# Kernel optimization log

Hardware: AMD Instinct MI355X
Metric: run time of the kernel (lower is better)

## Reference

```python
import jax, jax.numpy as jnp
import numpy as np

RES = 32


def _normalize_coords(coords, R):
    # coords: [B, 3, N] -> norm_coords in [0, R-1] (PVCNN Voxelization, normalize=True, eps=0)
    c = coords - coords.mean(axis=2, keepdims=True)
    scale = jnp.linalg.norm(c, axis=1, keepdims=True).max(axis=2, keepdims=True) * 2.0  # [B,1,1]
    c = c / scale + 0.5
    return jnp.clip(c * R, 0.0, R - 1.0)


def avg_voxelize(features, coords, R):
    # features: [B, C, N], coords: [B, 3, N] -> vox [B, C, R^3], norm_coords [B, 3, N]
    norm_coords = _normalize_coords(coords, R)
    vc = jnp.round(norm_coords).astype(jnp.int32)  # [B, 3, N]
    flat = (vc[:, 0] * R + vc[:, 1]) * R + vc[:, 2]  # [B, N]

    def per_batch(f, idx):
        sums = jax.ops.segment_sum(f.T, idx, num_segments=R ** 3)  # [R^3, C]
        cnt = jax.ops.segment_sum(jnp.ones(idx.shape, f.dtype), idx, num_segments=R ** 3)  # [R^3]
        return (sums / jnp.maximum(cnt, 1.0)[:, None]).T  # [C, R^3]

    vox = jax.vmap(per_batch)(features, flat)
    return vox, norm_coords


def trilinear_devoxelize(vox, coords, R):
    # vox: [B, C, R^3], coords: [B, 3, N] floats in [0, R-1]
    B, C, _ = vox.shape
    N = coords.shape[2]
    lo_f = jnp.floor(coords)
    d = coords - lo_f  # fractional part [B, 3, N]
    lo = lo_f.astype(jnp.int32)
    hi = jnp.minimum(lo + 1, R - 1)
    out = jnp.zeros((B, C, N), vox.dtype)
    for dx in (0, 1):
        for dy in (0, 1):
            for dz in (0, 1):
                ix = hi[:, 0] if dx else lo[:, 0]
                iy = hi[:, 1] if dy else lo[:, 1]
                iz = hi[:, 2] if dz else lo[:, 2]
                wx = d[:, 0] if dx else 1.0 - d[:, 0]
                wy = d[:, 1] if dy else 1.0 - d[:, 1]
                wz = d[:, 2] if dz else 1.0 - d[:, 2]
                w = wx * wy * wz  # [B, N]
                idx = (ix * R + iy) * R + iz  # [B, N]
                g = jnp.take_along_axis(vox, jnp.broadcast_to(idx[:, None, :], (B, C, N)), axis=2)
                out = out + w[:, None, :] * g
    return out


def setup_inputs() -> dict:
    key = jax.random.key(0)
    k1, k2, k3, k4 = jax.random.split(key, 4)
    B, C, N = 8, 64, 65536
    return {
        'x1_features': jax.random.normal(k1, (B, C, N), jnp.float32),
        'x2_features': jax.random.normal(k2, (B, C, N), jnp.float32),
        'x1_coords': jax.random.uniform(k3, (B, 3, N), jnp.float32),
        'x2_coords': jax.random.uniform(k4, (B, 3, N), jnp.float32),
    }


def reference(x1_features, x2_features, x1_coords, x2_coords):
    R = RES
    _vox_x1, nc_x1 = avg_voxelize(x1_features, x1_coords, R)
    vox_x2, _nc_x2 = avg_voxelize(x2_features, x2_coords, R)
    devox_mixed = trilinear_devoxelize(vox_x2, nc_x1, R)
    return jnp.concatenate([x1_features, devox_mixed], axis=1)
```

## Files before the change

kernel.cpp:

```cpp
#include <hip/hip_runtime.h>

namespace {
constexpr int R   = 32;
constexpr int R3  = R * R * R;
constexpr int NB  = 8;
constexpr int NC  = 64;
constexpr int NP  = 65536;

constexpr size_t OFF_SUM = 0;
constexpr size_t OFF_MAX = 512;
constexpr size_t OFF_CNT = 1024;
constexpr size_t OFF_VOX = OFF_CNT + sizeof(float) * (size_t)NB * R3;
constexpr size_t WS_BYTES = OFF_VOX + sizeof(float) * (size_t)NB * R3 * NC;

typedef float vfloat4 __attribute__((ext_vector_type(4)));
}

__device__ inline double wave_sum(double v) {
#pragma unroll
  for (int o = 32; o > 0; o >>= 1) v += __shfl_down(v, o, 64);
  return v;
}
__device__ inline double wave_max(double v) {
#pragma unroll
  for (int o = 32; o > 0; o >>= 1) v = fmax(v, __shfl_down(v, o, 64));
  return v;
}

__global__ __launch_bounds__(256) void k_sum(const float* __restrict__ c1,
                                             const float* __restrict__ c2,
                                             double* __restrict__ sums) {
  constexpr int CH = 32;
  int blk = blockIdx.x;
  int chunk = blk % CH; blk /= CH;
  int axis  = blk % 3;  blk /= 3;
  int b     = blk % NB; blk /= NB;
  int set   = blk;
  const float* src = (set == 0 ? c1 : c2) + ((size_t)b * 3 + axis) * NP;
  constexpr int PER = NP / CH;
  int base = chunk * PER;
  double s = 0.0;
  for (int i = threadIdx.x; i < PER; i += 256) s += (double)src[base + i];
  s = wave_sum(s);
  __shared__ double red[4];
  if ((threadIdx.x & 63) == 0) red[threadIdx.x >> 6] = s;
  __syncthreads();
  if (threadIdx.x == 0) {
    double t = red[0] + red[1] + red[2] + red[3];
    atomicAdd(&sums[((size_t)set * NB + b) * 3 + axis], t);
  }
}

__global__ __launch_bounds__(256) void k_max(const float* __restrict__ c1,
                                             const float* __restrict__ c2,
                                             const double* __restrict__ sums,
                                             unsigned long long* __restrict__ maxs) {
  constexpr int CH = 64;
  int blk = blockIdx.x;
  int chunk = blk % CH; blk /= CH;
  int b     = blk % NB; blk /= NB;
  int set   = blk;
  const float* src = (set == 0 ? c1 : c2) + (size_t)b * 3 * NP;
  const double invN = 1.0 / (double)NP;
  double m0 = sums[((size_t)set * NB + b) * 3 + 0] * invN;
  double m1 = sums[((size_t)set * NB + b) * 3 + 1] * invN;
  double m2 = sums[((size_t)set * NB + b) * 3 + 2] * invN;
  constexpr int PER = NP / CH;
  int base = chunk * PER;
  double mx = 0.0;
  for (int i = threadIdx.x; i < PER; i += 256) {
    int p = base + i;
    double x = (double)src[p] - m0;
    double y = (double)src[NP + p] - m1;
    double z = (double)src[2 * NP + p] - m2;
    mx = fmax(mx, x * x + y * y + z * z);
  }
  mx = wave_max(mx);
  __shared__ double red[4];
  if ((threadIdx.x & 63) == 0) red[threadIdx.x >> 6] = mx;
  __syncthreads();
  if (threadIdx.x == 0) {
    double t = fmax(fmax(red[0], red[1]), fmax(red[2], red[3]));
    atomicMax(&maxs[set * NB + b], (unsigned long long)__double_as_longlong(t));
  }
}

__global__ __launch_bounds__(256) void k_vox(const float* __restrict__ f2,
                                             const float* __restrict__ c2,
                                             const float* __restrict__ f1,
                                             const double* __restrict__ sums,
                                             const unsigned long long* __restrict__ maxs,
                                             float* __restrict__ counts,
                                             float* __restrict__ vox,
                                             float* __restrict__ out) {
  int lin = blockIdx.x;
  int b = lin & 7;
  int t = lin >> 3;
  int q = t / 5, r = t - q * 5;
  int tid = threadIdx.x;

  if (r == 4) {
    int p0c = q * 256;
    int w = tid >> 6, lane = tid & 63;
    const vfloat4* s4 = (const vfloat4*)(f1 + (size_t)b * NC * NP + p0c);
    vfloat4*       d4 = (vfloat4*)(out + (size_t)b * 2 * NC * NP + p0c);
#pragma unroll
    for (int rr = 0; rr < 16; ++rr) {
      int c = w * 16 + rr;
      size_t off = (size_t)c * (NP / 4) + lane;
      __builtin_nontemporal_store(__builtin_nontemporal_load(s4 + off), d4 + off);
    }
    return;
  }

  int p0 = (q * 4 + r) * 64;
  __shared__ int   s_idx[64];
  __shared__ float s_tile[64 * 65];

  if (tid < 64) {
    int p = p0 + tid;
    const double invN = 1.0 / (double)NP;
    double scale = 2.0 * sqrt(__longlong_as_double((long long)maxs[NB + b]));
    double inv = 1.0 / scale;
    const float* cb = c2 + (size_t)b * 3 * NP;
    int vc[3];
#pragma unroll
    for (int a = 0; a < 3; a++) {
      double mean = sums[((size_t)NB + b) * 3 + a] * invN;
      double nc = (((double)cb[a * NP + p] - mean) * inv + 0.5) * (double)R;
      nc = fmin(fmax(nc, 0.0), (double)(R - 1));
      vc[a] = (int)rint(nc);
    }
    int idx = (vc[0] * R + vc[1]) * R + vc[2];
    s_idx[tid] = idx;
    atomicAdd(&counts[(size_t)b * R3 + idx], 1.0f);
  }
  __syncthreads();

  const float* fb = f2 + (size_t)b * NC * NP;
#pragma unroll
  for (int i = 0; i < 16; i++) {
    int lin2 = i * 256 + tid;
    int c = lin2 >> 6, pl = lin2 & 63;
    s_tile[pl * 65 + c] = __builtin_nontemporal_load(&fb[(size_t)c * NP + p0 + pl]);
  }
  __syncthreads();

  int w = tid >> 6, lane = tid & 63;
  float* voxb = vox + (size_t)b * R3 * NC;
  for (int j = 0; j < 16; j++) {
    int pl = w * 16 + j;
    atomicAdd(&voxb[(size_t)s_idx[pl] * NC + lane], s_tile[pl * 65 + lane]);
  }
}

__global__ __launch_bounds__(256) void k_devox(const float* __restrict__ c1,
                                               const double* __restrict__ sums,
                                               const unsigned long long* __restrict__ maxs,
                                               const float* __restrict__ counts,
                                               const float* __restrict__ vox,
                                               float* __restrict__ out) {
  int lin = blockIdx.x;
  int b = lin & 7;
  int p0 = (lin >> 3) * 64;
  __shared__ int   s_idx[64][8];
  __shared__ float s_w[64][8];
  __shared__ float s_tile[64 * 65];
  int tid = threadIdx.x;

  if (tid < 64) {
    int p = p0 + tid;
    const double invN = 1.0 / (double)NP;
    double scale = 2.0 * sqrt(__longlong_as_double((long long)maxs[b]));
    double inv = 1.0 / scale;
    const float* cb = c1 + (size_t)b * 3 * NP;
    double nc[3];
#pragma unroll
    for (int a = 0; a < 3; a++) {
      double mean = sums[(size_t)b * 3 + a] * invN;
      double v = (((double)cb[a * NP + p] - mean) * inv + 0.5) * (double)R;
      nc[a] = fmin(fmax(v, 0.0), (double)(R - 1));
    }
    int lo[3], hi[3];
    double d[3];
#pragma unroll
    for (int a = 0; a < 3; a++) {
      lo[a] = (int)floor(nc[a]);
      d[a]  = nc[a] - (double)lo[a];
      hi[a] = min(lo[a] + 1, R - 1);
    }
    const float* cntb = counts + (size_t)b * R3;
#pragma unroll
    for (int k = 0; k < 8; k++) {
      int ix = (k & 4) ? hi[0] : lo[0];
      int iy = (k & 2) ? hi[1] : lo[1];
      int iz = (k & 1) ? hi[2] : lo[2];
      double wx = (k & 4) ? d[0] : 1.0 - d[0];
      double wy = (k & 2) ? d[1] : 1.0 - d[1];
      double wz = (k & 1) ? d[2] : 1.0 - d[2];
      int idx = (ix * R + iy) * R + iz;
      float cnt = cntb[idx];
      s_idx[tid][k] = idx;
      s_w[tid][k]   = (float)(wx * wy * wz) / fmaxf(cnt, 1.0f);
    }
  }
  __syncthreads();

  const float* voxb = vox + (size_t)b * R3 * NC;
  int w = tid >> 6, lane = tid & 63;
  for (int j = 0; j < 16; j++) {
    int pl = w * 16 + j;
    float acc = 0.0f;
#pragma unroll
    for (int k = 0; k < 8; k++) {
      acc += s_w[pl][k] * voxb[(size_t)s_idx[pl][k] * NC + lane];
    }
    s_tile[pl * 65 + lane] = acc;
  }
  __syncthreads();

  float* outb = out + (size_t)b * (2 * NC) * NP;
#pragma unroll
  for (int i = 0; i < 16; i++) {
    int lin2 = i * 256 + tid;
    int c = lin2 >> 6, pl = lin2 & 63;
    size_t pcol = (size_t)p0 + pl;
    __builtin_nontemporal_store(s_tile[pl * 65 + c], &outb[(size_t)(NC + c) * NP + pcol]);
  }
}

extern "C" void kernel_launch(void* const* d_in, const int* in_sizes, int n_in,
                              void* d_out, int out_size, void* d_ws, size_t ws_size,
                              hipStream_t stream) {
  const float* x1f = (const float*)d_in[0];
  const float* x2f = (const float*)d_in[1];
  const float* x1c = (const float*)d_in[2];
  const float* x2c = (const float*)d_in[3];
  float* out = (float*)d_out;

  char* ws = (char*)d_ws;
  double* sums             = (double*)(ws + OFF_SUM);
  unsigned long long* maxs = (unsigned long long*)(ws + OFF_MAX);
  float* cnts              = (float*)(ws + OFF_CNT);
  float* vox               = (float*)(ws + OFF_VOX);

  (void)hipMemsetAsync(ws, 0, WS_BYTES, stream);
  k_sum<<<2 * NB * 3 * 32, 256, 0, stream>>>(x1c, x2c, sums);
  k_max<<<2 * NB * 64, 256, 0, stream>>>(x1c, x2c, sums, maxs);
  k_vox<<<NB * (NP / 64 + NP / 256), 256, 0, stream>>>(x2f, x2c, x1f, sums, maxs, cnts, vox, out);
  k_devox<<<NB * (NP / 64), 256, 0, stream>>>(x1c, sums, maxs, cnts, vox, out);
}
```

Before: 585.1 us.

## Replace atomic voxel accumulation with counting-sort scatter and per-voxel reduction

Voxelization no longer uses float atomicAdd into the voxel grid. The new path computes voxel indices and integer counts, prefix-scans the counts per batch, scatters point features into voxel-sorted order, and then sums each voxel's contiguous run to produce the mean. The averaging moves into the reduce step, and the x1 feature copy moves into the devox kernel. This aims to cut atomic contention on hot voxels, at the cost of an extra 128MB write plus read of the sorted feature buffer, more kernel launches, and a serial per-voxel loop that is imbalanced when voxel counts are skewed.

```diff
diff --git a/kernel.cpp b/kernel.cpp
--- a/kernel.cpp
+++ b/kernel.cpp
@@ -10,8 +10,12 @@
 constexpr size_t OFF_SUM = 0;
 constexpr size_t OFF_MAX = 512;
 constexpr size_t OFF_CNT = 1024;
-constexpr size_t OFF_VOX = OFF_CNT + sizeof(float) * (size_t)NB * R3;
-constexpr size_t WS_BYTES = OFF_VOX + sizeof(float) * (size_t)NB * R3 * NC;
+constexpr size_t OFF_OFF = OFF_CNT + sizeof(int) * (size_t)NB * R3;
+constexpr size_t OFF_CUR = OFF_OFF + sizeof(int) * (size_t)NB * R3;
+constexpr size_t OFF_IDX = OFF_CUR + sizeof(int) * (size_t)NB * R3;
+constexpr size_t OFF_VOX = OFF_IDX + sizeof(int) * (size_t)NB * NP;
+constexpr size_t OFF_FT  = OFF_VOX + sizeof(float) * (size_t)NB * R3 * NC;
+constexpr size_t WS_BYTES = OFF_FT + sizeof(float) * (size_t)NB * NP * NC;
 
 typedef float vfloat4 __attribute__((ext_vector_type(4)));
 }
@@ -85,14 +89,122 @@
   }
 }
 
-__global__ __launch_bounds__(256) void k_vox(const float* __restrict__ f2,
-                                             const float* __restrict__ c2,
-                                             const float* __restrict__ f1,
+__global__ __launch_bounds__(256) void k_idx(const float* __restrict__ c2,
                                              const double* __restrict__ sums,
                                              const unsigned long long* __restrict__ maxs,
-                                             float* __restrict__ counts,
-                                             float* __restrict__ vox,
-                                             float* __restrict__ out) {
+                                             int* __restrict__ counts,
+                                             int* __restrict__ idxArr) {
+  int lin = blockIdx.x;
+  int b = lin & 7;
+  int p0 = (lin >> 3) * 1024;
+  const double invN = 1.0 / (double)NP;
+  double scale = 2.0 * sqrt(__longlong_as_double((long long)maxs[NB + b]));
+  double inv = 1.0 / scale;
+  double m0 = sums[((size_t)NB + b) * 3 + 0] * invN;
+  double m1 = sums[((size_t)NB + b) * 3 + 1] * invN;
+  double m2 = sums[((size_t)NB + b) * 3 + 2] * invN;
+  const float* cb = c2 + (size_t)b * 3 * NP;
+#pragma unroll
+  for (int k = 0; k < 4; k++) {
+    int p = p0 + k * 256 + threadIdx.x;
+    double n0 = (((double)cb[p] - m0) * inv + 0.5) * (double)R;
+    double n1 = (((double)cb[NP + p] - m1) * inv + 0.5) * (double)R;
+    double n2 = (((double)cb[2 * NP + p] - m2) * inv + 0.5) * (double)R;
+    n0 = fmin(fmax(n0, 0.0), (double)(R - 1));
+    n1 = fmin(fmax(n1, 0.0), (double)(R - 1));
+    n2 = fmin(fmax(n2, 0.0), (double)(R - 1));
+    int id = ((int)rint(n0) * R + (int)rint(n1)) * R + (int)rint(n2);
+    idxArr[(size_t)b * NP + p] = id;
+    atomicAdd(&counts[(size_t)b * R3 + id], 1);
+  }
+}
+
+__global__ __launch_bounds__(1024) void k_prefix(const int* __restrict__ counts,
+                                                 int* __restrict__ offs,
+                                                 int* __restrict__ cur) {
+  int b = blockIdx.x;
+  int t = threadIdx.x;
+  int lane = t & 63, w = t >> 6;
+  __shared__ int wtot[16];
+  int base = b * R3 + t * 32;
+  int c[32]; int s = 0;
+#pragma unroll
+  for (int k = 0; k < 32; k++) { c[k] = counts[base + k]; s += c[k]; }
+  int v = s;
+#pragma unroll
+  for (int o = 1; o < 64; o <<= 1) { int u = __shfl_up(v, o, 64); if (lane >= o) v += u; }
+  if (lane == 63) wtot[w] = v;
+  __syncthreads();
+  if (w == 0) {
+    int x = (lane < 16) ? wtot[lane] : 0;
+#pragma unroll
+    for (int o = 1; o < 16; o <<= 1) { int u = __shfl_up(x, o, 64); if (lane >= o) x += u; }
+    if (lane < 16) wtot[lane] = x;
+  }
+  __syncthreads();
+  int run = v - s + (w > 0 ? wtot[w - 1] : 0);
+#pragma unroll
+  for (int k = 0; k < 32; k++) { offs[base + k] = run; cur[base + k] = run; run += c[k]; }
+}
+
+__global__ __launch_bounds__(256) void k_scatter(const float* __restrict__ f2,
+                                                 const int* __restrict__ idxArr,
+                                                 int* __restrict__ cur,
+                                                 float* __restrict__ fT) {
+  int lin = blockIdx.x;
+  int b = lin & 7;
+  int p0 = (lin >> 3) * 64;
+  int tid = threadIdx.x;
+  __shared__ int   s_pos[64];
+  __shared__ float s_tile[64 * 65];
+
+  if (tid < 64) {
+    int id = idxArr[(size_t)b * NP + p0 + tid];
+    s_pos[tid] = atomicAdd(&cur[(size_t)b * R3 + id], 1);
+  }
+  __syncthreads();
+
+  const float* fb = f2 + (size_t)b * NC * NP;
+#pragma unroll
+  for (int i = 0; i < 16; i++) {
+    int l2 = i * 256 + tid;
+    int c = l2 >> 6, pl = l2 & 63;
+    s_tile[pl * 65 + c] = __builtin_nontemporal_load(&fb[(size_t)c * NP + p0 + pl]);
+  }
+  __syncthreads();
+
+  int w = tid >> 6, lane = tid & 63;
+  float* ftb = fT + (size_t)b * NP * NC;
+  for (int j = 0; j < 16; j++) {
+    int pl = w * 16 + j;
+    ftb[(size_t)s_pos[pl] * NC + lane] = s_tile[pl * 65 + lane];
+  }
+}
+
+__global__ __launch_bounds__(256) void k_reduce(const int* __restrict__ counts,
+                                                const int* __restrict__ offs,
+                                                const float* __restrict__ fT,
+                                                float* __restrict__ vox) {
+  int lin = blockIdx.x;
+  int b = lin & 7;
+  int v = (lin >> 3) * 4 + (threadIdx.x >> 6);
+  int lane = threadIdx.x & 63;
+  int off = offs[(size_t)b * R3 + v];
+  int cnt = counts[(size_t)b * R3 + v];
+  const float* ftb = fT + (size_t)b * NP * NC;
+  float acc = 0.0f;
+  for (int i = 0; i < cnt; i++)
+    acc += __builtin_nontemporal_load(&ftb[(size_t)(off + i) * NC + lane]);
+  float m = (cnt > 0) ? acc / (float)cnt : 0.0f;
+  vox[((size_t)b * R3 + v) * NC + lane] = m;
+}
+
+__global__ __launch_bounds__(256) void k_devox(const float* __restrict__ c1,
+                                               const double* __restrict__ sums,
+                                               const unsigned long long* __restrict__ maxs,
+                                               const float* __restrict__ vox,
+                                               const float* __restrict__ f1,
+                                               float* __restrict__ out) {
   int lin = blockIdx.x;
   int b = lin & 7;
   int t = lin >> 3;
@@ -114,59 +226,9 @@
   }
 
   int p0 = (q * 4 + r) * 64;
-  __shared__ int   s_idx[64];
-  __shared__ float s_tile[64 * 65];
-
-  if (tid < 64) {
-    int p = p0 + tid;
-    const double invN = 1.0 / (double)NP;
-    double scale = 2.0 * sqrt(__longlong_as_double((long long)maxs[NB + b]));
-    double inv = 1.0 / scale;
-    const float* cb = c2 + (size_t)b * 3 * NP;
-    int vc[3];
-#pragma unroll
-    for (int a = 0; a < 3; a++) {
-      double mean = sums[((size_t)NB + b) * 3 + a] * invN;
-      double nc = (((double)cb[a * NP + p] - mean) * inv + 0.5) * (double)R;
-      nc = fmin(fmax(nc, 0.0), (double)(R - 1));
-      vc[a] = (int)rint(nc);
-    }
-    int idx = (vc[0] * R + vc[1]) * R + vc[2];
-    s_idx[tid] = idx;
-    atomicAdd(&counts[(size_t)b * R3 + idx], 1.0f);
-  }
-  __syncthreads();
-
-  const float* fb = f2 + (size_t)b * NC * NP;
-#pragma unroll
-  for (int i = 0; i < 16; i++) {
-    int lin2 = i * 256 + tid;
-    int c = lin2 >> 6, pl = lin2 & 63;
-    s_tile[pl * 65 + c] = __builtin_nontemporal_load(&fb[(size_t)c * NP + p0 + pl]);
-  }
-  __syncthreads();
-
-  int w = tid >> 6, lane = tid & 63;
-  float* voxb = vox + (size_t)b * R3 * NC;
-  for (int j = 0; j < 16; j++) {
-    int pl = w * 16 + j;
-    atomicAdd(&voxb[(size_t)s_idx[pl] * NC + lane], s_tile[pl * 65 + lane]);
-  }
-}
-
-__global__ __launch_bounds__(256) void k_devox(const float* __restrict__ c1,
-                                               const double* __restrict__ sums,
-                                               const unsigned long long* __restrict__ maxs,
-                                               const float* __restrict__ counts,
-                                               const float* __restrict__ vox,
-                                               float* __restrict__ out) {
-  int lin = blockIdx.x;
-  int b = lin & 7;
-  int p0 = (lin >> 3) * 64;
   __shared__ int   s_idx[64][8];
   __shared__ float s_w[64][8];
   __shared__ float s_tile[64 * 65];
-  int tid = threadIdx.x;
 
   if (tid < 64) {
     int p = p0 + tid;
@@ -189,7 +251,6 @@
       d[a]  = nc[a] - (double)lo[a];
       hi[a] = min(lo[a] + 1, R - 1);
     }
-    const float* cntb = counts + (size_t)b * R3;
 #pragma unroll
     for (int k = 0; k < 8; k++) {
       int ix = (k & 4) ? hi[0] : lo[0];
@@ -198,10 +259,8 @@
       double wx = (k & 4) ? d[0] : 1.0 - d[0];
       double wy = (k & 2) ? d[1] : 1.0 - d[1];
       double wz = (k & 1) ? d[2] : 1.0 - d[2];
-      int idx = (ix * R + iy) * R + iz;
-      float cnt = cntb[idx];
-      s_idx[tid][k] = idx;
-      s_w[tid][k]   = (float)(wx * wy * wz) / fmaxf(cnt, 1.0f);
+      s_idx[tid][k] = (ix * R + iy) * R + iz;
+      s_w[tid][k]   = (float)(wx * wy * wz);
     }
   }
   __syncthreads();
@@ -222,8 +281,8 @@
   float* outb = out + (size_t)b * (2 * NC) * NP;
 #pragma unroll
   for (int i = 0; i < 16; i++) {
-    int lin2 = i * 256 + tid;
-    int c = lin2 >> 6, pl = lin2 & 63;
+    int l2 = i * 256 + tid;
+    int c = l2 >> 6, pl = l2 & 63;
     size_t pcol = (size_t)p0 + pl;
     __builtin_nontemporal_store(s_tile[pl * 65 + c], &outb[(size_t)(NC + c) * NP + pcol]);
   }
@@ -241,12 +300,19 @@
   char* ws = (char*)d_ws;
   double* sums             = (double*)(ws + OFF_SUM);
   unsigned long long* maxs = (unsigned long long*)(ws + OFF_MAX);
-  float* cnts              = (float*)(ws + OFF_CNT);
+  int* cnts                = (int*)(ws + OFF_CNT);
+  int* offs                = (int*)(ws + OFF_OFF);
+  int* cur                 = (int*)(ws + OFF_CUR);
+  int* idxA                = (int*)(ws + OFF_IDX);
   float* vox               = (float*)(ws + OFF_VOX);
-
-  (void)hipMemsetAsync(ws, 0, WS_BYTES, stream);
+  float* fT                = (float*)(ws + OFF_FT);
+
+  (void)hipMemsetAsync(ws, 0, OFF_OFF, stream);
   k_sum<<<2 * NB * 3 * 32, 256, 0, stream>>>(x1c, x2c, sums);
   k_max<<<2 * NB * 64, 256, 0, stream>>>(x1c, x2c, sums, maxs);
-  k_vox<<<NB * (NP / 64 + NP / 256), 256, 0, stream>>>(x2f, x2c, x1f, sums, maxs, cnts, vox, out);
-  k_devox<<<NB * (NP / 64), 256, 0, stream>>>(x1c, sums, maxs, cnts, vox, out);
-}
+  k_idx<<<NB * (NP / 1024), 256, 0, stream>>>(x2c, sums, maxs, cnts, idxA);
+  k_prefix<<<NB, 1024, 0, stream>>>(cnts, offs, cur);
+  k_scatter<<<NB * (NP / 64), 256, 0, stream>>>(x2f, idxA, cur, fT);
+  k_reduce<<<NB * (R3 / 4), 256, 0, stream>>>(cnts, offs, fT, vox);
+  k_devox<<<NB * (NP / 64 + NP / 256), 256, 0, stream>>>(x1c, sums, maxs, vox, x1f, out);
+}
```

Result: slower. 598.1 us (+2.2%).
